# Kernel tuning notes

Measured on AMD Instinct MI355X. Metric: run time of the kernel, lower is better.

## Reference

```python
import jax, jax.numpy as jnp
import numpy as np

K = 9      # kernel_size
H = 6      # num_head
HD = 64    # head_dim
D = H * HD # reduced_hidden_dim = 384
B, S = 16, 1024
OUT = 384  # hidden_dim // 2


def setup_inputs() -> dict:
    key = jax.random.key(0)
    k = jax.random.split(key, 5)
    q = jax.random.normal(k[0], (B, S, D), dtype=jnp.float32)
    ks = jax.random.normal(k[1], (B, S, D), dtype=jnp.float32)
    v = jax.random.normal(k[2], (B, S, D), dtype=jnp.float32)
    Wk = jax.random.normal(k[3], (K * H, D), dtype=jnp.float32) * 0.02
    bk = jnp.zeros((K * H,), dtype=jnp.float32)
    Wp = jax.random.normal(k[4], (OUT, D), dtype=jnp.float32) * 0.02
    bp = jnp.zeros((OUT,), dtype=jnp.float32)
    return {"q": q, "ks": ks, "v": v, "Wk": Wk, "bk": bk, "Wp": Wp, "bp": bp}


def reference(q, ks, v, Wk, bk, Wp, bp):
    b, s, d = v.shape
    pad = K // 2
    # expand4conv: zero-pad along seq and gather K-wide sliding windows
    vp = jnp.pad(v, ((0, 0), (pad, pad), (0, 0)))            # [B, S+K-1, D]
    win = jnp.stack([vp[:, i:i + s] for i in range(K)], -1)  # [B, S, D, K]
    win = win.reshape(b, s, H, HD, K)                        # [B, S, H, HD, K]
    # dynamic kernel: softmax over kernel taps
    logits = jnp.einsum('bsd,od->bso', q * ks, Wk) + bk       # [B, S, K*H]
    dk = jax.nn.softmax(logits.reshape(b, s, H, K), axis=-1)  # [B, S, H, K]
    # local weighted reduction over the window
    out = jnp.einsum('bshdk,bshk->bshd', win, dk).reshape(b, s, d)
    return jnp.einsum('bsd,od->bso', out, Wp) + bp            # [B, S, OUT]
```

## Files before the change

### kernel.cpp

```cpp
#include <hip/hip_runtime.h>
#include <hip/hip_bf16.h>

#define BB 16
#define SS 1024
#define DD 384
#define HH 6
#define KK 9
#define KH 54
#define OUTD 384
#define NKT 12
#define VLD 392

typedef __attribute__((ext_vector_type(4))) float floatx4;
typedef __attribute__((ext_vector_type(8))) __bf16 bf16x8;
typedef __attribute__((ext_vector_type(4))) __bf16 bf16x4;

__global__ __launch_bounds__(256) void cast_kernel(const float* __restrict__ Wk,
                                                   const float* __restrict__ Wp,
                                                   __bf16* __restrict__ WkT,
                                                   __bf16* __restrict__ WpT) {
    int i = blockIdx.x * 256 + threadIdx.x;
    if (i < 4 * NKT * 64 * 8) {
        int e = i & 7, lane = (i >> 3) & 63, t = i >> 9;
        int kstep = t % NKT, ntile = t / NKT;
        int row = ntile * 16 + (lane & 15);
        int col = kstep * 32 + ((lane >> 4) << 3) + e;
        WkT[i] = (row < KH) ? (__bf16)Wk[row * DD + col] : (__bf16)0.0f;
    } else if (i < 24576 + 24 * NKT * 64 * 8) {
        int j = i - 24576;
        int e = j & 7, lane = (j >> 3) & 63, t = j >> 9;
        int kstep = t % NKT, ntile = t / NKT;
        int row = ntile * 16 + (lane & 15);
        int col = kstep * 32 + ((lane >> 4) << 3) + e;
        WpT[j] = (__bf16)Wp[row * DD + col];
    }
}

__global__ __launch_bounds__(256, 4) void fused_kernel(const float* __restrict__ q,
                                                       const float* __restrict__ ks,
                                                       const float* __restrict__ v,
                                                       const __bf16* __restrict__ WkT,
                                                       const float* __restrict__ bk,
                                                       const __bf16* __restrict__ WpT,
                                                       const float* __restrict__ bp,
                                                       float* __restrict__ out) {
    __shared__ __bf16 vqS[40 * VLD];
    __shared__ float  dkS[16 * 56];
    __shared__ float  lgS[16 * 66];

    const int tid  = threadIdx.x;
    const int wave = tid >> 6;
    const int lane = tid & 63;
    const int m0   = blockIdx.x * 16;
    const int b    = blockIdx.x >> 6;
    const int s0   = (blockIdx.x & 63) * 16;
    const int fr   = lane & 15;
    const int fk   = (lane >> 4) * 8;
    const int col_in = lane & 15;
    const int rgrp   = (lane >> 4) * 4;

    __bf16* aS = &vqS[0];

    {
        const float* qb = q  + (size_t)m0 * DD;
        const float* kb = ks + (size_t)m0 * DD;
#pragma unroll
        for (int it = 0; it < 6; ++it) {
            int c = tid + it * 256;
            int row = c / 96, col = (c % 96) * 4;
            floatx4 qv = *reinterpret_cast<const floatx4*>(qb + (size_t)row * DD + col);
            floatx4 kv = *reinterpret_cast<const floatx4*>(kb + (size_t)row * DD + col);
            floatx4 pr = qv * kv;
            bf16x4 pk = { (__bf16)pr.x, (__bf16)pr.y, (__bf16)pr.z, (__bf16)pr.w };
            *reinterpret_cast<bf16x4*>(&vqS[row * VLD + col]) = pk;
        }
        const float* vb = v + (size_t)b * SS * DD;
        if (s0 != 0 && s0 != SS - 16) {
#pragma unroll
            for (int it = 0; it < 9; ++it) {
                int c = tid + it * 256;
                int row = c / 96, col = (c % 96) * 4;
                floatx4 val = *reinterpret_cast<const floatx4*>(
                    vb + (size_t)(s0 + row - 4) * DD + col);
                bf16x4 vk = { (__bf16)val.x, (__bf16)val.y, (__bf16)val.z, (__bf16)val.w };
                *reinterpret_cast<bf16x4*>(&vqS[(16 + row) * VLD + col]) = vk;
            }
        } else {
#pragma unroll
            for (int it = 0; it < 9; ++it) {
                int c = tid + it * 256;
                int row = c / 96, col = (c % 96) * 4;
                int r = s0 + row - 4;
                floatx4 val = {};
                if (r >= 0 && r < SS)
                    val = *reinterpret_cast<const floatx4*>(vb + (size_t)r * DD + col);
                bf16x4 vk = { (__bf16)val.x, (__bf16)val.y, (__bf16)val.z, (__bf16)val.w };
                *reinterpret_cast<bf16x4*>(&vqS[(16 + row) * VLD + col]) = vk;
            }
        }
    }
    __syncthreads();

    {
        floatx4 acc = {};
#pragma unroll
        for (int s = 0; s < NKT; ++s) {
            bf16x8 af = *reinterpret_cast<const bf16x8*>(&vqS[fr * VLD + s * 32 + fk]);
            bf16x8 bf = *reinterpret_cast<const bf16x8*>(
                WkT + (((wave * NKT + s) * 64 + lane) << 3));
            acc = __builtin_amdgcn_mfma_f32_16x16x32_bf16(af, bf, acc, 0, 0, 0);
        }
#pragma unroll
        for (int r = 0; r < 4; ++r)
            lgS[(rgrp + r) * 66 + wave * 16 + col_in] = acc[r];
    }
    __syncthreads();

    if (tid < 16 * HH) {
        int row = tid / HH, h = tid % HH;
        float lg[KK];
        float mx = -1e30f;
#pragma unroll
        for (int k = 0; k < KK; ++k) {
            float s = lgS[row * 66 + h * KK + k] + bk[h * KK + k];
            lg[k] = s;
            mx = fmaxf(mx, s);
        }
        float sum = 0.0f;
#pragma unroll
        for (int k = 0; k < KK; ++k) { lg[k] = __expf(lg[k] - mx); sum += lg[k]; }
        float inv = 1.0f / sum;
#pragma unroll
        for (int k = 0; k < KK; ++k) dkS[row * 56 + h * KK + k] = lg[k] * inv;
    }
    __syncthreads();

#pragma unroll
    for (int it = 0; it < 6; ++it) {
        int p = tid + it * 256;
        int row = p / 96, c4 = p % 96;
        int h = c4 >> 4;
        const float* dkr = &dkS[row * 56 + h * KK];
        floatx4 a = {};
#pragma unroll
        for (int k = 0; k < KK; ++k) {
            bf16x4 w = *reinterpret_cast<const bf16x4*>(&vqS[(16 + row + k) * VLD + c4 * 4]);
            floatx4 wf = { (float)w[0], (float)w[1], (float)w[2], (float)w[3] };
            a += wf * dkr[k];
        }
        bf16x4 o = { (__bf16)a.x, (__bf16)a.y, (__bf16)a.z, (__bf16)a.w };
        *reinterpret_cast<bf16x4*>(&aS[row * VLD + c4 * 4]) = o;
    }
    __syncthreads();

    {
        const int nt0 = wave * 6;
        floatx4 acc[6] = {};
#pragma unroll
        for (int s = 0; s < NKT; ++s) {
            bf16x8 af = *reinterpret_cast<const bf16x8*>(&aS[fr * VLD + s * 32 + fk]);
#pragma unroll
            for (int j = 0; j < 6; ++j) {
                bf16x8 bf = *reinterpret_cast<const bf16x8*>(
                    WpT + ((((nt0 + j) * NKT + s) * 64 + lane) << 3));
                acc[j] = __builtin_amdgcn_mfma_f32_16x16x32_bf16(af, bf, acc[j], 0, 0, 0);
            }
        }
        float* ob = out + (size_t)m0 * OUTD;
#pragma unroll
        for (int j = 0; j < 6; ++j) {
            int col = (nt0 + j) * 16 + col_in;
            float bv = bp[col];
#pragma unroll
            for (int r = 0; r < 4; ++r)
                ob[(size_t)(rgrp + r) * OUTD + col] = acc[j][r] + bv;
        }
    }
}

extern "C" void kernel_launch(void* const* d_in, const int* in_sizes, int n_in,
                              void* d_out, int out_size, void* d_ws, size_t ws_size,
                              hipStream_t stream) {
    const float* q  = (const float*)d_in[0];
    const float* ks = (const float*)d_in[1];
    const float* v  = (const float*)d_in[2];
    const float* Wk = (const float*)d_in[3];
    const float* bk = (const float*)d_in[4];
    const float* Wp = (const float*)d_in[5];
    const float* bp = (const float*)d_in[6];
    float* out = (float*)d_out;

    __bf16* WkT = (__bf16*)d_ws;
    __bf16* WpT = (__bf16*)((char*)d_ws + 49152);

    cast_kernel<<<(24576 + 147456 + 255) / 256, 256, 0, stream>>>(Wk, Wp, WkT, WpT);
    fused_kernel<<<(BB * SS) / 16, 256, 0, stream>>>(q, ks, v, WkT, bk, WpT, bp, out);
}
```

Baseline: 127.0 us.

## Split fused kernel into two stages with bf16 intermediate in MFMA fragment layout

```diff
diff --git a/kernel.cpp b/kernel.cpp
--- a/kernel.cpp
+++ b/kernel.cpp
@@ -36,15 +36,14 @@
     }
 }
 
-__global__ __launch_bounds__(256, 4) void fused_kernel(const float* __restrict__ q,
-                                                       const float* __restrict__ ks,
-                                                       const float* __restrict__ v,
-                                                       const __bf16* __restrict__ WkT,
-                                                       const float* __restrict__ bk,
-                                                       const __bf16* __restrict__ WpT,
-                                                       const float* __restrict__ bp,
-                                                       float* __restrict__ out) {
-    __shared__ __bf16 vqS[40 * VLD];
+__global__ __launch_bounds__(256, 4) void stage1_kernel(const float* __restrict__ q,
+                                                        const float* __restrict__ ks,
+                                                        const float* __restrict__ v,
+                                                        const __bf16* __restrict__ WkT,
+                                                        const float* __restrict__ bk,
+                                                        __bf16* __restrict__ Aws) {
+    __shared__ __bf16 qkS[16 * VLD];
+    __shared__ __bf16 vS[24 * VLD];
     __shared__ float  dkS[16 * 56];
     __shared__ float  lgS[16 * 66];
 
@@ -59,8 +58,6 @@
     const int col_in = lane & 15;
     const int rgrp   = (lane >> 4) * 4;
 
-    __bf16* aS = &vqS[0];
-
     {
         const float* qb = q  + (size_t)m0 * DD;
         const float* kb = ks + (size_t)m0 * DD;
@@ -72,7 +69,7 @@
             floatx4 kv = *reinterpret_cast<const floatx4*>(kb + (size_t)row * DD + col);
             floatx4 pr = qv * kv;
             bf16x4 pk = { (__bf16)pr.x, (__bf16)pr.y, (__bf16)pr.z, (__bf16)pr.w };
-            *reinterpret_cast<bf16x4*>(&vqS[row * VLD + col]) = pk;
+            *reinterpret_cast<bf16x4*>(&qkS[row * VLD + col]) = pk;
         }
         const float* vb = v + (size_t)b * SS * DD;
         if (s0 != 0 && s0 != SS - 16) {
@@ -83,7 +80,7 @@
                 floatx4 val = *reinterpret_cast<const floatx4*>(
                     vb + (size_t)(s0 + row - 4) * DD + col);
                 bf16x4 vk = { (__bf16)val.x, (__bf16)val.y, (__bf16)val.z, (__bf16)val.w };
-                *reinterpret_cast<bf16x4*>(&vqS[(16 + row) * VLD + col]) = vk;
+                *reinterpret_cast<bf16x4*>(&vS[row * VLD + col]) = vk;
             }
         } else {
 #pragma unroll
@@ -95,7 +92,7 @@
                 if (r >= 0 && r < SS)
                     val = *reinterpret_cast<const floatx4*>(vb + (size_t)r * DD + col);
                 bf16x4 vk = { (__bf16)val.x, (__bf16)val.y, (__bf16)val.z, (__bf16)val.w };
-                *reinterpret_cast<bf16x4*>(&vqS[(16 + row) * VLD + col]) = vk;
+                *reinterpret_cast<bf16x4*>(&vS[row * VLD + col]) = vk;
             }
         }
     }
@@ -105,7 +102,7 @@
         floatx4 acc = {};
 #pragma unroll
         for (int s = 0; s < NKT; ++s) {
-            bf16x8 af = *reinterpret_cast<const bf16x8*>(&vqS[fr * VLD + s * 32 + fk]);
+            bf16x8 af = *reinterpret_cast<const bf16x8*>(&qkS[fr * VLD + s * 32 + fk]);
             bf16x8 bf = *reinterpret_cast<const bf16x8*>(
                 WkT + (((wave * NKT + s) * 64 + lane) << 3));
             acc = __builtin_amdgcn_mfma_f32_16x16x32_bf16(af, bf, acc, 0, 0, 0);
@@ -135,46 +132,63 @@
     }
     __syncthreads();
 
-#pragma unroll
-    for (int it = 0; it < 6; ++it) {
+    __bf16* ab = Aws + ((size_t)blockIdx.x * NKT * 64) * 8;
+#pragma unroll
+    for (int it = 0; it < 3; ++it) {
         int p = tid + it * 256;
-        int row = p / 96, c4 = p % 96;
-        int h = c4 >> 4;
+        int s  = p >> 6, ln = p & 63;
+        int row = ln & 15, d0 = s * 32 + ((ln >> 4) << 3);
+        int h = d0 >> 6;
         const float* dkr = &dkS[row * 56 + h * KK];
-        floatx4 a = {};
+        float a[8] = {};
 #pragma unroll
         for (int k = 0; k < KK; ++k) {
-            bf16x4 w = *reinterpret_cast<const bf16x4*>(&vqS[(16 + row + k) * VLD + c4 * 4]);
-            floatx4 wf = { (float)w[0], (float)w[1], (float)w[2], (float)w[3] };
-            a += wf * dkr[k];
-        }
-        bf16x4 o = { (__bf16)a.x, (__bf16)a.y, (__bf16)a.z, (__bf16)a.w };
-        *reinterpret_cast<bf16x4*>(&aS[row * VLD + c4 * 4]) = o;
-    }
-    __syncthreads();
-
-    {
-        const int nt0 = wave * 6;
-        floatx4 acc[6] = {};
-#pragma unroll
-        for (int s = 0; s < NKT; ++s) {
-            bf16x8 af = *reinterpret_cast<const bf16x8*>(&aS[fr * VLD + s * 32 + fk]);
-#pragma unroll
-            for (int j = 0; j < 6; ++j) {
-                bf16x8 bf = *reinterpret_cast<const bf16x8*>(
-                    WpT + ((((nt0 + j) * NKT + s) * 64 + lane) << 3));
-                acc[j] = __builtin_amdgcn_mfma_f32_16x16x32_bf16(af, bf, acc[j], 0, 0, 0);
-            }
-        }
-        float* ob = out + (size_t)m0 * OUTD;
+            bf16x8 w = *reinterpret_cast<const bf16x8*>(&vS[(row + k) * VLD + d0]);
+            float dv = dkr[k];
+#pragma unroll
+            for (int e = 0; e < 8; ++e) a[e] += (float)w[e] * dv;
+        }
+        bf16x8 o;
+#pragma unroll
+        for (int e = 0; e < 8; ++e) o[e] = (__bf16)a[e];
+        *reinterpret_cast<bf16x8*>(&ab[(size_t)(s * 64 + ln) * 8]) = o;
+    }
+}
+
+__global__ __launch_bounds__(256) void stage2_kernel(const __bf16* __restrict__ Aws,
+                                                     const __bf16* __restrict__ WpT,
+                                                     const float* __restrict__ bp,
+                                                     float* __restrict__ out) {
+    const int tid   = threadIdx.x;
+    const int wave  = tid >> 6;
+    const int lane  = tid & 63;
+    const int w     = blockIdx.x * 4 + wave;
+    const int mtile = w >> 2;
+    const int colq  = w & 3;
+    const int col_in = lane & 15;
+    const int rgrp   = (lane >> 4) * 4;
+
+    floatx4 acc[6] = {};
+#pragma unroll
+    for (int s = 0; s < NKT; ++s) {
+        bf16x8 af = *reinterpret_cast<const bf16x8*>(
+            Aws + (((size_t)(mtile * NKT + s) * 64 + lane) << 3));
 #pragma unroll
         for (int j = 0; j < 6; ++j) {
-            int col = (nt0 + j) * 16 + col_in;
-            float bv = bp[col];
-#pragma unroll
-            for (int r = 0; r < 4; ++r)
-                ob[(size_t)(rgrp + r) * OUTD + col] = acc[j][r] + bv;
-        }
+            bf16x8 bf = *reinterpret_cast<const bf16x8*>(
+                WpT + ((((colq * 6 + j) * NKT + s) * 64 + lane) << 3));
+            acc[j] = __builtin_amdgcn_mfma_f32_16x16x32_bf16(af, bf, acc[j], 0, 0, 0);
+        }
+    }
+
+    float* ob = out + (size_t)mtile * 16 * OUTD;
+#pragma unroll
+    for (int j = 0; j < 6; ++j) {
+        int col = (colq * 6 + j) * 16 + col_in;
+        float bv = bp[col];
+#pragma unroll
+        for (int r = 0; r < 4; ++r)
+            ob[(size_t)(rgrp + r) * OUTD + col] = acc[j][r] + bv;
     }
 }
 
@@ -192,7 +206,9 @@
 
     __bf16* WkT = (__bf16*)d_ws;
     __bf16* WpT = (__bf16*)((char*)d_ws + 49152);
+    __bf16* Aws = (__bf16*)((char*)d_ws + 49152 + 294912);
 
     cast_kernel<<<(24576 + 147456 + 255) / 256, 256, 0, stream>>>(Wk, Wp, WkT, WpT);
-    fused_kernel<<<(BB * SS) / 16, 256, 0, stream>>>(q, ks, v, WkT, bk, WpT, bp, out);
-}
+    stage1_kernel<<<(BB * SS) / 16, 256, 0, stream>>>(q, ks, v, WkT, bk, Aws);
+    stage2_kernel<<<(BB * SS) / 16, 256, 0, stream>>>(Aws, WpT, bp, out);
+}
```

Measured after the change: 137.1 us. 1.08x slower.
